# Optimization experiments

Hardware: AMD Instinct MI355X
Metric: run time of the kernel (lower is better)

## Reference

```python
import jax, jax.numpy as jnp
import numpy as np

B, T, D, E = 2, 1653, 512, 8
D_E = D // E
BE = B * E


def setup_inputs() -> dict:
    key = jax.random.key(0)
    ks = jax.random.split(key, 11)
    s = 0.02  # keep linear-layer scale sane
    return {
        "input": jax.random.normal(ks[0], (B, T, D), jnp.float32),
        "Wq": jax.random.normal(ks[1], (D, D), jnp.float32) * s,
        "bq": jax.random.normal(ks[2], (D,), jnp.float32) * s,
        "Wk": jax.random.normal(ks[3], (D, D), jnp.float32) * s,
        "bk": jax.random.normal(ks[4], (D,), jnp.float32) * s,
        "Wv": jax.random.normal(ks[5], (D, D), jnp.float32) * s,
        "bv": jax.random.normal(ks[6], (D,), jnp.float32) * s,
        "Wo": jax.random.normal(ks[7], (D, D), jnp.float32) * s,
        "bo": jax.random.normal(ks[8], (D,), jnp.float32) * s,
        # random 'gaussian orthogonal punishment' matrix (diag(norms) @ blockwise-QR in torch; random here)
        "punish": jax.random.normal(ks[9], (T, T), jnp.float32) * (1.0 / np.sqrt(T)),
        # random tensor produced by torch.nn.init.orthogonal_(att_score) in the source
        "att_orth": jax.random.normal(ks[10], (BE, T, T), jnp.float32) * (1.0 / np.sqrt(T)),
    }


def _learnable_sigmoid(x):
    return 1.2 / (1.0 + jnp.exp(-1.6 * x))


def reference(input, Wq, bq, Wk, bk, Wv, bv, Wo, bo, punish, att_orth):
    # torch nn.Linear: y = x @ W^T + b
    def proj(W, b):
        # [B,T,D] -> permute(0,2,1) -> [B,D,T] -> reshape to [B*E, T, D_E]
        y = jnp.einsum('btd,ed->bte', input, W) + b
        return y.transpose(0, 2, 1).reshape(BE, T, D_E)

    Q = _learnable_sigmoid(proj(Wq, bq))            # [BE, T, D_E] (mask_q is all-ones => no-op)
    K = _learnable_sigmoid(proj(Wk, bk))            # [BE, T, D_E]
    V = proj(Wv, bv)                                # [BE, T, D_E]

    inv_sqrt_T = 1.0 / jnp.sqrt(jnp.float32(T))
    att = jnp.einsum('btd,bsd->bts', Q, K) * inv_sqrt_T  # [BE, T, T]

    # punishment: elementwise mul by broadcast punish matrix, then matmul with
    # the (transposed) random orthogonal tensor: att = (att * P) @ orth^T
    att = (att * punish[None, :, :]) @ att_orth.transpose(0, 2, 1)  # [BE, T, T]

    att = jnp.where(att == 0.0, jnp.float32(-2e20), att)  # masked_fill(att==0, -2e20)

    out = jnp.einsum('bts,bsd->btd', att, V)        # [BE, T, D_E]
    # permute(0,2,1) -> [BE, D_E, T] -> reshape [B, D, T] -> permute -> [B, T, D]
    out = out.transpose(0, 2, 1).reshape(B, D, T).transpose(0, 2, 1)
    return jnp.einsum('btd,ed->bte', out, Wo) + bo   # [B, T, D]
```

## Files before the change

kernel.cpp:

```cpp
#include <hip/hip_runtime.h>

#define TT 1653
#define DD 512
#define BB 2
#define DE 64
#define BEH 16
#define TTILES 26
#define TPAD 1664
#define SQN 26
#define NJC 4
#define MPSTRIDE TPAD

typedef __attribute__((ext_vector_type(8))) short bf16x8;
typedef __attribute__((ext_vector_type(4))) float f32x4;
typedef short bf16x8u __attribute__((ext_vector_type(8), aligned(4)));
typedef float f32x4u  __attribute__((ext_vector_type(4), aligned(4)));

__device__ __forceinline__ short f2bf(float f) {
    union { float f; unsigned u; } v; v.f = f;
    unsigned r = v.u + 0x7fffu + ((v.u >> 16) & 1u);
    return (short)(r >> 16);
}
__device__ __forceinline__ unsigned pack2(float a, float b) {
    return (unsigned)(unsigned short)f2bf(a) | ((unsigned)(unsigned short)f2bf(b) << 16);
}
__device__ __forceinline__ float bf2f(short s) {
    union { unsigned u; float f; } v; v.u = ((unsigned)(unsigned short)s) << 16;
    return v.f;
}
__device__ __forceinline__ bf16x8 ld_frag4(const short* p) {
    bf16x8u v = *(const bf16x8u*)p;
    return (bf16x8)v;
}

__global__ __launch_bounds__(256) void convp2_kernel(
    const float* __restrict__ P, short* __restrict__ Pbf)
{
    const int g = blockIdx.x * 256 + threadIdx.x;
    const int NG4 = TPAD / 4;
    if (g >= TT * NG4) return;
    const int r = g / NG4, c4 = (g - r * NG4) * 4;
    float p0 = 0.f, p1 = 0.f, p2 = 0.f, p3 = 0.f;
    const float* prow = P + (size_t)r * TT;
    if (c4 + 0 < TT) p0 = prow[c4 + 0];
    if (c4 + 1 < TT) p1 = prow[c4 + 1];
    if (c4 + 2 < TT) p2 = prow[c4 + 2];
    if (c4 + 3 < TT) p3 = prow[c4 + 3];
    uint2 o; o.x = pack2(p0, p1); o.y = pack2(p2, p3);
    *(uint2*)(Pbf + (size_t)r * TPAD + c4) = o;
}

__global__ __launch_bounds__(256) void proj2_kernel(
    const float* __restrict__ X,
    const float* __restrict__ W0, const float* __restrict__ b0,
    const float* __restrict__ W1, const float* __restrict__ b1,
    const float* __restrict__ W2, const float* __restrict__ b2,
    short* __restrict__ Y0, short* __restrict__ Y1, short* __restrict__ Y2)
{
    __shared__ short Wsh[64][72];
    __shared__ short Xs[64][72];

    const int tt = blockIdx.x, dt = blockIdx.y, z = blockIdx.z;
    const int b = z / 3, which = z % 3;
    const float* W    = (which == 0) ? W0 : (which == 1) ? W1 : W2;
    const float* bias = (which == 0) ? b0 : (which == 1) ? b1 : b2;
    short* Y          = (which == 0) ? Y0 : (which == 1) ? Y1 : Y2;

    const int t0 = tt * 64, d0 = dt * 64;
    const float* Xb = X + (size_t)b * TT * DD;

    const int tid  = threadIdx.x;
    const int wave = tid >> 6, lane = tid & 63;
    const int quad = lane >> 4, l16 = lane & 15;
    const int srow = tid >> 2, scg = (tid & 3) * 16;

    f32x4 acc[4];
    #pragma unroll
    for (int i = 0; i < 4; ++i) acc[i] = (f32x4){0.f, 0.f, 0.f, 0.f};

    for (int k0 = 0; k0 < DD; k0 += 64) {
        {
            const float* wrow = W + (size_t)(d0 + srow) * DD + k0 + scg;
            float4 w0 = *(const float4*)(wrow);
            float4 w1 = *(const float4*)(wrow + 4);
            float4 w2 = *(const float4*)(wrow + 8);
            float4 w3 = *(const float4*)(wrow + 12);
            uint4 pw0, pw1;
            pw0.x = pack2(w0.x, w0.y); pw0.y = pack2(w0.z, w0.w);
            pw0.z = pack2(w1.x, w1.y); pw0.w = pack2(w1.z, w1.w);
            pw1.x = pack2(w2.x, w2.y); pw1.y = pack2(w2.z, w2.w);
            pw1.z = pack2(w3.x, w3.y); pw1.w = pack2(w3.z, w3.w);

            const int t = t0 + srow;
            float4 x0 = make_float4(0.f,0.f,0.f,0.f), x1 = x0, x2 = x0, x3 = x0;
            if (t < TT) {
                const float* xrow = Xb + (size_t)t * DD + k0 + scg;
                x0 = *(const float4*)(xrow);
                x1 = *(const float4*)(xrow + 4);
                x2 = *(const float4*)(xrow + 8);
                x3 = *(const float4*)(xrow + 12);
            }
            uint4 px0, px1;
            px0.x = pack2(x0.x, x0.y); px0.y = pack2(x0.z, x0.w);
            px0.z = pack2(x1.x, x1.y); px0.w = pack2(x1.z, x1.w);
            px1.x = pack2(x2.x, x2.y); px1.y = pack2(x2.z, x2.w);
            px1.z = pack2(x3.x, x3.y); px1.w = pack2(x3.z, x3.w);

            __syncthreads();
            *(uint4*)&Wsh[srow][scg]     = pw0;
            *(uint4*)&Wsh[srow][scg + 8] = pw1;
            *(uint4*)&Xs[srow][scg]      = px0;
            *(uint4*)&Xs[srow][scg + 8]  = px1;
        }
        __syncthreads();

        #pragma unroll
        for (int ks = 0; ks < 2; ++ks) {
            bf16x8 a = *(const bf16x8*)&Wsh[wave * 16 + l16][ks * 32 + quad * 8];
            #pragma unroll
            for (int nt = 0; nt < 4; ++nt) {
                bf16x8 bb = *(const bf16x8*)&Xs[nt * 16 + l16][ks * 32 + quad * 8];
                acc[nt] = __builtin_amdgcn_mfma_f32_16x16x32_bf16(a, bb, acc[nt], 0, 0, 0);
            }
        }
    }

    #pragma unroll
    for (int nt = 0; nt < 4; ++nt) {
        const int t = t0 + nt * 16 + l16;
        if (t < TT) {
            #pragma unroll
            for (int r = 0; r < 4; ++r) {
                const int d = d0 + wave * 16 + quad * 4 + r;
                float v = acc[nt][r] + bias[d];
                if (which < 2) v = 1.2f / (1.0f + __expf(-1.6f * v));
                Y[((size_t)b * DD + d) * TT + t] = f2bf(v);
            }
        }
    }
}

__global__ __launch_bounds__(256, 6) void ovt4_kernel(
    const float* __restrict__ orth, const short* __restrict__ Vb,
    float* __restrict__ Mpart)
{
    __shared__ short Os[64][66];
    __shared__ short Vs[64][66];

    const int sq = blockIdx.x, be = blockIdx.y, jc = blockIdx.z;
    const int s0 = sq * 64;
    const int jt0 = (jc < 2) ? jc * 7 : 14 + (jc - 2) * 6;
    const int jtn = (jc < 2) ? 7 : 6;

    const float* O  = orth + (size_t)be * TT * TT;
    const short* Vh = Vb + (size_t)be * DE * TT;

    const int tid  = threadIdx.x;
    const int wave = tid >> 6, lane = tid & 63;
    const int quad = lane >> 4, l16 = lane & 15;

    const int c4 = tid & 15;
    const int pr = tid >> 4;
    const int ca = s0 + 4 * c4;
    const bool fastS = (s0 + 64 <= TT);

    f32x4 acc[4];
    #pragma unroll
    for (int i = 0; i < 4; ++i) acc[i] = (f32x4){0.f, 0.f, 0.f, 0.f};

    f32x4u o0a, o0b, o1a, o1b;
    uint2  v0a, v0b, v1a, v1b;

    auto stage_load = [&](int j0) {
        const int jA0 = j0 + 2 * pr;
        const int jA1 = jA0 + 32;
        const int r0  = min(jA0,     TT - 1);
        const int r0b = min(jA0 + 1, TT - 1);
        const int r1  = min(jA1,     TT - 1);
        const int r1b = min(jA1 + 1, TT - 1);
        if (fastS) {
            o0a = *(const f32x4u*)(O + (size_t)r0  * TT + ca);
            o0b = *(const f32x4u*)(O + (size_t)r0b * TT + ca);
            o1a = *(const f32x4u*)(O + (size_t)r1  * TT + ca);
            o1b = *(const f32x4u*)(O + (size_t)r1b * TT + ca);
        } else {
            #pragma unroll
            for (int i = 0; i < 4; ++i) {
                const int col = ca + i;
                const bool cv = (col < TT);
                o0a[i] = cv ? O[(size_t)r0  * TT + col] : 0.f;
                o0b[i] = cv ? O[(size_t)r0b * TT + col] : 0.f;
                o1a[i] = cv ? O[(size_t)r1  * TT + col] : 0.f;
                o1b[i] = cv ? O[(size_t)r1b * TT + col] : 0.f;
            }
        }
        const uint2 z = make_uint2(0u, 0u);
        v0a = (jA0     < TT) ? *(const uint2*)(Vh + (size_t)jA0       * DE + 4 * c4) : z;
        v0b = (jA0 + 1 < TT) ? *(const uint2*)(Vh + (size_t)(jA0 + 1) * DE + 4 * c4) : z;
        v1a = (jA1     < TT) ? *(const uint2*)(Vh + (size_t)jA1       * DE + 4 * c4) : z;
        v1b = (jA1 + 1 < TT) ? *(const uint2*)(Vh + (size_t)(jA1 + 1) * DE + 4 * c4) : z;
    };

    auto lds_write = [&]() {
        #pragma unroll
        for (int i = 0; i < 4; ++i) {
            *(unsigned*)&Os[4 * c4 + i][2 * pr]      = pack2(o0a[i], o0b[i]);
            *(unsigned*)&Os[4 * c4 + i][2 * pr + 32] = pack2(o1a[i], o1b[i]);
        }
        *(unsigned*)&Vs[4 * c4 + 0][2 * pr]      = (v0a.x & 0xffffu) | (v0b.x << 16);
        *(unsigned*)&Vs[4 * c4 + 1][2 * pr]      = (v0a.x >> 16)     | (v0b.x & 0xffff0000u);
        *(unsigned*)&Vs[4 * c4 + 2][2 * pr]      = (v0a.y & 0xffffu) | (v0b.y << 16);
        *(unsigned*)&Vs[4 * c4 + 3][2 * pr]      = (v0a.y >> 16)     | (v0b.y & 0xffff0000u);
        *(unsigned*)&Vs[4 * c4 + 0][2 * pr + 32] = (v1a.x & 0xffffu) | (v1b.x << 16);
        *(unsigned*)&Vs[4 * c4 + 1][2 * pr + 32] = (v1a.x >> 16)     | (v1b.x & 0xffff0000u);
        *(unsigned*)&Vs[4 * c4 + 2][2 * pr + 32] = (v1a.y & 0xffffu) | (v1b.y << 16);
        *(unsigned*)&Vs[4 * c4 + 3][2 * pr + 32] = (v1a.y >> 16)     | (v1b.y & 0xffff0000u);
    };

    stage_load(jt0 * 64);
    for (int t = 0; t < jtn; ++t) {
        if (t) __syncthreads();
        lds_write();
        if (t + 1 < jtn) stage_load((jt0 + t + 1) * 64);
        __syncthreads();
        #pragma unroll
        for (int ks = 0; ks < 2; ++ks) {
            bf16x8 bb = ld_frag4(&Os[wave * 16 + l16][ks * 32 + quad * 8]);
            #pragma unroll
            for (int i = 0; i < 4; ++i) {
                bf16x8 a = ld_frag4(&Vs[i * 16 + l16][ks * 32 + quad * 8]);
                acc[i] = __builtin_amdgcn_mfma_f32_16x16x32_bf16(a, bb, acc[i], 0, 0, 0);
            }
        }
    }

    float* Mp = Mpart + (size_t)(jc * BEH + be) * DE * MPSTRIDE;
    const int s = s0 + wave * 16 + l16;
    #pragma unroll
    for (int i = 0; i < 4; ++i) {
        #pragma unroll
        for (int r = 0; r < 4; ++r) {
            const int d = i * 16 + quad * 4 + r;
            Mp[(size_t)d * MPSTRIDE + s] = acc[i][r];
        }
    }
}

__global__ __launch_bounds__(256) void mreduce_kernel(
    const float* __restrict__ Mpart, short* __restrict__ Mt)
{
    const int g = blockIdx.x * 256 + threadIdx.x;
    const int NG = TPAD / 4;
    if (g >= BEH * DE * NG) return;
    const int bd = g / NG;
    const int s4 = (g - bd * NG) * 4;

    const size_t jstride = (size_t)BEH * DE * MPSTRIDE;
    const float* p = Mpart + (size_t)bd * MPSTRIDE + s4;
    float4 a0 = *(const float4*)(p);
    float4 a1 = *(const float4*)(p + jstride);
    float4 a2 = *(const float4*)(p + 2 * jstride);
    float4 a3 = *(const float4*)(p + 3 * jstride);
    float s0 = a0.x + a1.x + a2.x + a3.x;
    float s1 = a0.y + a1.y + a2.y + a3.y;
    float s2 = a0.z + a1.z + a2.z + a3.z;
    float s3 = a0.w + a1.w + a2.w + a3.w;

    uint2 o;
    o.x = pack2(s0, s1);
    o.y = pack2(s2, s3);
    *(uint2*)(Mt + (size_t)bd * TPAD + s4) = o;
}

__global__ __launch_bounds__(256) void attn2_kernel(
    const short* __restrict__ Qb, const short* __restrict__ Kb,
    const short* __restrict__ Mt, const short* __restrict__ Pbf,
    float* __restrict__ Hbuf)
{
    __shared__ short Qs[64][72];
    __shared__ short Ks[64][72];
    __shared__ short Ms[64][72];
    __shared__ short Wl[64][72];
    __shared__ short Ps[64][72];

    const int it = blockIdx.x, be = blockIdx.y;
    const int b = be >> 3, e = be & 7;
    const int i0 = it * 64;
    const short* Qh = Qb + (size_t)be * DE * TT;
    const short* Kh = Kb + (size_t)be * DE * TT;
    const short* Mh = Mt + (size_t)be * DE * TPAD;

    const int tid  = threadIdx.x;
    const int wave = tid >> 6, lane = tid & 63;
    const int quad = lane >> 4, l16 = lane & 15;

    const float invs = 0.024598297f;

    const int srow = tid >> 2, scg = (tid & 3) * 16;

    {
        const int gi = i0 + srow;
        uint4 z = make_uint4(0u, 0u, 0u, 0u);
        uint4 v0 = z, v1 = z;
        if (gi < TT) {
            v0 = *(const uint4*)(Qh + (size_t)gi * DE + scg);
            v1 = *(const uint4*)(Qh + (size_t)gi * DE + scg + 8);
        }
        *(uint4*)&Qs[srow][scg]     = v0;
        *(uint4*)&Qs[srow][scg + 8] = v1;
    }

    f32x4 out[4];
    #pragma unroll
    for (int i = 0; i < 4; ++i) out[i] = (f32x4){0.f, 0.f, 0.f, 0.f};

    for (int s0 = 0; s0 < TT; s0 += 64) {
        {
            const int gs = s0 + srow;
            uint4 z = make_uint4(0u, 0u, 0u, 0u);
            uint4 k0 = z, k1 = z;
            if (gs < TT) {
                k0 = *(const uint4*)(Kh + (size_t)gs * DE + scg);
                k1 = *(const uint4*)(Kh + (size_t)gs * DE + scg + 8);
            }
            *(uint4*)&Ks[srow][scg]     = k0;
            *(uint4*)&Ks[srow][scg + 8] = k1;

            uint4 m0 = *(const uint4*)(Mh + (size_t)srow * TPAD + s0 + scg);
            uint4 m1 = *(const uint4*)(Mh + (size_t)srow * TPAD + s0 + scg + 8);
            *(uint4*)&Ms[srow][scg]     = m0;
            *(uint4*)&Ms[srow][scg + 8] = m1;

            const int gi = i0 + srow;
            uint4 p0 = z, p1 = z;
            if (gi < TT) {
                p0 = *(const uint4*)(Pbf + (size_t)gi * TPAD + s0 + scg);
                p1 = *(const uint4*)(Pbf + (size_t)gi * TPAD + s0 + scg + 8);
            }
            *(uint4*)&Ps[srow][scg]     = p0;
            *(uint4*)&Ps[srow][scg + 8] = p1;
        }
        __syncthreads();

        f32x4 w[4];
        #pragma unroll
        for (int i = 0; i < 4; ++i) w[i] = (f32x4){0.f, 0.f, 0.f, 0.f};
        #pragma unroll
        for (int ks = 0; ks < 2; ++ks) {
            bf16x8 a = *(const bf16x8*)&Qs[wave * 16 + l16][ks * 32 + quad * 8];
            #pragma unroll
            for (int stile = 0; stile < 4; ++stile) {
                bf16x8 bb = *(const bf16x8*)&Ks[stile * 16 + l16][ks * 32 + quad * 8];
                w[stile] = __builtin_amdgcn_mfma_f32_16x16x32_bf16(a, bb, w[stile], 0, 0, 0);
            }
        }

        #pragma unroll
        for (int stile = 0; stile < 4; ++stile) {
            const int sl = stile * 16 + l16;
            #pragma unroll
            for (int r = 0; r < 4; ++r) {
                const int il = wave * 16 + quad * 4 + r;
                float v = w[stile][r] * invs * bf2f(Ps[il][sl]);
                Wl[il][sl] = f2bf(v);
            }
        }

        #pragma unroll
        for (int ks = 0; ks < 2; ++ks) {
            bf16x8 a = *(const bf16x8*)&Wl[wave * 16 + l16][ks * 32 + quad * 8];
            #pragma unroll
            for (int dt = 0; dt < 4; ++dt) {
                bf16x8 bb = *(const bf16x8*)&Ms[dt * 16 + l16][ks * 32 + quad * 8];
                out[dt] = __builtin_amdgcn_mfma_f32_16x16x32_bf16(a, bb, out[dt], 0, 0, 0);
            }
        }
        __syncthreads();
    }

    #pragma unroll
    for (int dt = 0; dt < 4; ++dt) {
        const int d = dt * 16 + l16;
        #pragma unroll
        for (int r = 0; r < 4; ++r) {
            const int gi = i0 + wave * 16 + quad * 4 + r;
            if (gi < TT)
                Hbuf[((size_t)b * TT + gi) * DD + e * 64 + d] = out[dt][r];
        }
    }
}

__global__ __launch_bounds__(256) void oproj_kernel(
    const float* __restrict__ H, const float* __restrict__ Wo,
    const float* __restrict__ bo, float* __restrict__ out)
{
    __shared__ float Hs[16][68];
    __shared__ float Ns[16][68];

    const int tt = blockIdx.x, nt = blockIdx.y, b = blockIdx.z;
    const int t0 = tt * 64, n0 = nt * 64;
    const float* Hb = H + (size_t)b * TT * DD;

    const int tid = threadIdx.x;
    const int tx = tid & 15, ty = tid >> 4;
    const int lrow = tid >> 2, lq = tid & 3;
    const int trow = t0 + lrow;

    float acc[4][4] = {};

    for (int k0 = 0; k0 < DD; k0 += 16) {
        float4 hv = make_float4(0.f, 0.f, 0.f, 0.f);
        if (trow < TT)
            hv = *(const float4*)(Hb + (size_t)trow * DD + k0 + lq*4);
        float4 wv = *(const float4*)(Wo + (size_t)(n0 + lrow) * DD + k0 + lq*4);
        __syncthreads();
        Hs[lq*4+0][lrow] = hv.x; Hs[lq*4+1][lrow] = hv.y;
        Hs[lq*4+2][lrow] = hv.z; Hs[lq*4+3][lrow] = hv.w;
        Ns[lq*4+0][lrow] = wv.x; Ns[lq*4+1][lrow] = wv.y;
        Ns[lq*4+2][lrow] = wv.z; Ns[lq*4+3][lrow] = wv.w;
        __syncthreads();
        #pragma unroll
        for (int k = 0; k < 16; ++k) {
            float4 a4 = *(const float4*)(&Hs[k][ty*4]);
            float4 c4 = *(const float4*)(&Ns[k][tx*4]);
            float a[4] = {a4.x, a4.y, a4.z, a4.w};
            float c[4] = {c4.x, c4.y, c4.z, c4.w};
            #pragma unroll
            for (int i = 0; i < 4; ++i)
                #pragma unroll
                for (int j = 0; j < 4; ++j)
                    acc[i][j] = fmaf(a[i], c[j], acc[i][j]);
        }
        __syncthreads();
    }

    #pragma unroll
    for (int i = 0; i < 4; ++i) {
        const int t = t0 + ty*4 + i;
        if (t < TT) {
            float4 v;
            v.x = acc[i][0] + bo[n0 + tx*4 + 0];
            v.y = acc[i][1] + bo[n0 + tx*4 + 1];
            v.z = acc[i][2] + bo[n0 + tx*4 + 2];
            v.w = acc[i][3] + bo[n0 + tx*4 + 3];
            *(float4*)(out + ((size_t)b * TT + t) * DD + n0 + tx*4) = v;
        }
    }
}

extern "C" void kernel_launch(void* const* d_in, const int* in_sizes, int n_in,
                              void* d_out, int out_size, void* d_ws, size_t ws_size,
                              hipStream_t stream)
{
    (void)in_sizes; (void)n_in; (void)out_size; (void)ws_size;

    const float* X    = (const float*)d_in[0];
    const float* Wq   = (const float*)d_in[1];
    const float* bq   = (const float*)d_in[2];
    const float* Wk   = (const float*)d_in[3];
    const float* bk   = (const float*)d_in[4];
    const float* Wv   = (const float*)d_in[5];
    const float* bv   = (const float*)d_in[6];
    const float* Wo   = (const float*)d_in[7];
    const float* bo   = (const float*)d_in[8];
    const float* P    = (const float*)d_in[9];
    const float* orth = (const float*)d_in[10];
    float* out = (float*)d_out;

    char* ws = (char*)d_ws;
    const size_t SZH = (size_t)BB * DD * TT * sizeof(short);
    short* Qb  = (short*)(ws);
    short* Kb  = (short*)(ws + SZH);
    short* Vb  = (short*)(ws + 2 * SZH);
    short* Mtb = (short*)(ws + 3 * SZH);
    short* Pbf = (short*)(ws + 3 * SZH + (size_t)BEH * DE * TPAD * sizeof(short));
    char*  after_p = ws + 3 * SZH + (size_t)BEH * DE * TPAD * sizeof(short)
                        + (size_t)TT * TPAD * sizeof(short);
    float* Mpart = (float*)after_p;
    float* Hbuf  = (float*)after_p;

    dim3 blk(256);

    convp2_kernel<<<dim3((TT * (TPAD / 4) + 255) / 256), blk, 0, stream>>>(P, Pbf);

    dim3 g1(TTILES, DD / 64, BB * 3);
    proj2_kernel<<<g1, blk, 0, stream>>>(X, Wq, bq, Wk, bk, Wv, bv, Qb, Kb, Vb);

    dim3 g2(SQN, BEH, NJC);
    ovt4_kernel<<<g2, blk, 0, stream>>>(orth, Vb, Mpart);

    dim3 gr((BEH * DE * (TPAD / 4) + 255) / 256);
    mreduce_kernel<<<gr, blk, 0, stream>>>(Mpart, Mtb);

    dim3 g3(TTILES, BEH);
    attn2_kernel<<<g3, blk, 0, stream>>>(Qb, Kb, Mtb, Pbf, Hbuf);

    dim3 g4(TTILES, DD / 64, BB);
    oproj_kernel<<<g4, blk, 0, stream>>>(Hbuf, Wo, bo, out);
}
```

Baseline: 409.4 us.

## Add register double-buffered prefetch to projection, OV and attention kernels

Each of the three main kernels now loads the next K-tile from global memory into registers while computing on the current tile. The OV kernel moves to a two-stage register ping-pong and relaxes launch bounds to 4 waves per SIMD. The attention kernel also gains two-stage register staging and drops the separate Wl LDS buffer by writing the scaled scores back into Ps. The aim is to hide global load latency and cut LDS footprint, at the cost of higher register pressure and lower occupancy.

```diff
diff --git a/kernel.cpp b/kernel.cpp
--- a/kernel.cpp
+++ b/kernel.cpp
@@ -13,7 +13,6 @@
 
 typedef __attribute__((ext_vector_type(8))) short bf16x8;
 typedef __attribute__((ext_vector_type(4))) float f32x4;
-typedef short bf16x8u __attribute__((ext_vector_type(8), aligned(4)));
 typedef float f32x4u  __attribute__((ext_vector_type(4), aligned(4)));
 
 __device__ __forceinline__ short f2bf(float f) {
@@ -27,10 +26,6 @@
 __device__ __forceinline__ float bf2f(short s) {
     union { unsigned u; float f; } v; v.u = ((unsigned)(unsigned short)s) << 16;
     return v.f;
-}
-__device__ __forceinline__ bf16x8 ld_frag4(const short* p) {
-    bf16x8u v = *(const bf16x8u*)p;
-    return (bf16x8)v;
 }
 
 __global__ __launch_bounds__(256) void convp2_kernel(
@@ -50,15 +45,15 @@
     *(uint2*)(Pbf + (size_t)r * TPAD + c4) = o;
 }
 
-__global__ __launch_bounds__(256) void proj2_kernel(
+__global__ __launch_bounds__(256) void proj3_kernel(
     const float* __restrict__ X,
     const float* __restrict__ W0, const float* __restrict__ b0,
     const float* __restrict__ W1, const float* __restrict__ b1,
     const float* __restrict__ W2, const float* __restrict__ b2,
     short* __restrict__ Y0, short* __restrict__ Y1, short* __restrict__ Y2)
 {
-    __shared__ short Wsh[64][72];
-    __shared__ short Xs[64][72];
+    __shared__ __align__(16) short Wsh[64][72];
+    __shared__ __align__(16) short Xs[64][72];
 
     const int tt = blockIdx.x, dt = blockIdx.y, z = blockIdx.z;
     const int b = z / 3, which = z % 3;
@@ -78,40 +73,45 @@
     #pragma unroll
     for (int i = 0; i < 4; ++i) acc[i] = (f32x4){0.f, 0.f, 0.f, 0.f};
 
+    float4 w0, w1, w2, w3, x0, x1, x2, x3;
+
+    auto stage = [&](int k0) {
+        const float* wrow = W + (size_t)(d0 + srow) * DD + k0 + scg;
+        w0 = *(const float4*)(wrow);
+        w1 = *(const float4*)(wrow + 4);
+        w2 = *(const float4*)(wrow + 8);
+        w3 = *(const float4*)(wrow + 12);
+        const int t = t0 + srow;
+        x0 = make_float4(0.f,0.f,0.f,0.f); x1 = x0; x2 = x0; x3 = x0;
+        if (t < TT) {
+            const float* xrow = Xb + (size_t)t * DD + k0 + scg;
+            x0 = *(const float4*)(xrow);
+            x1 = *(const float4*)(xrow + 4);
+            x2 = *(const float4*)(xrow + 8);
+            x3 = *(const float4*)(xrow + 12);
+        }
+    };
+    auto lds_write = [&]() {
+        uint4 pw0, pw1, px0, px1;
+        pw0.x = pack2(w0.x, w0.y); pw0.y = pack2(w0.z, w0.w);
+        pw0.z = pack2(w1.x, w1.y); pw0.w = pack2(w1.z, w1.w);
+        pw1.x = pack2(w2.x, w2.y); pw1.y = pack2(w2.z, w2.w);
+        pw1.z = pack2(w3.x, w3.y); pw1.w = pack2(w3.z, w3.w);
+        px0.x = pack2(x0.x, x0.y); px0.y = pack2(x0.z, x0.w);
+        px0.z = pack2(x1.x, x1.y); px0.w = pack2(x1.z, x1.w);
+        px1.x = pack2(x2.x, x2.y); px1.y = pack2(x2.z, x2.w);
+        px1.z = pack2(x3.x, x3.y); px1.w = pack2(x3.z, x3.w);
+        *(uint4*)&Wsh[srow][scg]     = pw0;
+        *(uint4*)&Wsh[srow][scg + 8] = pw1;
+        *(uint4*)&Xs[srow][scg]      = px0;
+        *(uint4*)&Xs[srow][scg + 8]  = px1;
+    };
+
+    stage(0);
     for (int k0 = 0; k0 < DD; k0 += 64) {
-        {
-            const float* wrow = W + (size_t)(d0 + srow) * DD + k0 + scg;
-            float4 w0 = *(const float4*)(wrow);
-            float4 w1 = *(const float4*)(wrow + 4);
-            float4 w2 = *(const float4*)(wrow + 8);
-            float4 w3 = *(const float4*)(wrow + 12);
-            uint4 pw0, pw1;
-            pw0.x = pack2(w0.x, w0.y); pw0.y = pack2(w0.z, w0.w);
-            pw0.z = pack2(w1.x, w1.y); pw0.w = pack2(w1.z, w1.w);
-            pw1.x = pack2(w2.x, w2.y); pw1.y = pack2(w2.z, w2.w);
-            pw1.z = pack2(w3.x, w3.y); pw1.w = pack2(w3.z, w3.w);
-
-            const int t = t0 + srow;
-            float4 x0 = make_float4(0.f,0.f,0.f,0.f), x1 = x0, x2 = x0, x3 = x0;
-            if (t < TT) {
-                const float* xrow = Xb + (size_t)t * DD + k0 + scg;
-                x0 = *(const float4*)(xrow);
-                x1 = *(const float4*)(xrow + 4);
-                x2 = *(const float4*)(xrow + 8);
-                x3 = *(const float4*)(xrow + 12);
-            }
-            uint4 px0, px1;
-            px0.x = pack2(x0.x, x0.y); px0.y = pack2(x0.z, x0.w);
-            px0.z = pack2(x1.x, x1.y); px0.w = pack2(x1.z, x1.w);
-            px1.x = pack2(x2.x, x2.y); px1.y = pack2(x2.z, x2.w);
-            px1.z = pack2(x3.x, x3.y); px1.w = pack2(x3.z, x3.w);
-
-            __syncthreads();
-            *(uint4*)&Wsh[srow][scg]     = pw0;
-            *(uint4*)&Wsh[srow][scg + 8] = pw1;
-            *(uint4*)&Xs[srow][scg]      = px0;
-            *(uint4*)&Xs[srow][scg + 8]  = px1;
-        }
+        if (k0) __syncthreads();
+        lds_write();
+        if (k0 + 64 < DD) stage(k0 + 64);
         __syncthreads();
 
         #pragma unroll
@@ -140,12 +140,17 @@
     }
 }
 
-__global__ __launch_bounds__(256, 6) void ovt4_kernel(
+struct OVStage {
+    f32x4u o0a, o0b, o1a, o1b;
+    uint2  v0a, v0b, v1a, v1b;
+};
+
+__global__ __launch_bounds__(256, 4) void ovt5_kernel(
     const float* __restrict__ orth, const short* __restrict__ Vb,
     float* __restrict__ Mpart)
 {
-    __shared__ short Os[64][66];
-    __shared__ short Vs[64][66];
+    __shared__ __align__(16) short Os[64][72];
+    __shared__ __align__(16) short Vs[64][72];
 
     const int sq = blockIdx.x, be = blockIdx.y, jc = blockIdx.z;
     const int s0 = sq * 64;
@@ -159,78 +164,88 @@
     const int wave = tid >> 6, lane = tid & 63;
     const int quad = lane >> 4, l16 = lane & 15;
 
-    const int c4 = tid & 15;
-    const int pr = tid >> 4;
-    const int ca = s0 + 4 * c4;
+    const int p  = tid & 15;
+    const int sc = tid >> 4;
+    const int ca = s0 + 4 * sc;
     const bool fastS = (s0 + 64 <= TT);
 
     f32x4 acc[4];
     #pragma unroll
     for (int i = 0; i < 4; ++i) acc[i] = (f32x4){0.f, 0.f, 0.f, 0.f};
 
-    f32x4u o0a, o0b, o1a, o1b;
-    uint2  v0a, v0b, v1a, v1b;
-
-    auto stage_load = [&](int j0) {
-        const int jA0 = j0 + 2 * pr;
-        const int jA1 = jA0 + 32;
-        const int r0  = min(jA0,     TT - 1);
-        const int r0b = min(jA0 + 1, TT - 1);
-        const int r1  = min(jA1,     TT - 1);
-        const int r1b = min(jA1 + 1, TT - 1);
+    auto stage_load = [&](OVStage& S, int j0) {
+        const int jA = j0 + 2 * p;
+        const int r0  = min(jA,      TT - 1);
+        const int r0b = min(jA + 1,  TT - 1);
+        const int r1  = min(jA + 32, TT - 1);
+        const int r1b = min(jA + 33, TT - 1);
         if (fastS) {
-            o0a = *(const f32x4u*)(O + (size_t)r0  * TT + ca);
-            o0b = *(const f32x4u*)(O + (size_t)r0b * TT + ca);
-            o1a = *(const f32x4u*)(O + (size_t)r1  * TT + ca);
-            o1b = *(const f32x4u*)(O + (size_t)r1b * TT + ca);
+            S.o0a = *(const f32x4u*)(O + (size_t)r0  * TT + ca);
+            S.o0b = *(const f32x4u*)(O + (size_t)r0b * TT + ca);
+            S.o1a = *(const f32x4u*)(O + (size_t)r1  * TT + ca);
+            S.o1b = *(const f32x4u*)(O + (size_t)r1b * TT + ca);
         } else {
             #pragma unroll
             for (int i = 0; i < 4; ++i) {
                 const int col = ca + i;
                 const bool cv = (col < TT);
-                o0a[i] = cv ? O[(size_t)r0  * TT + col] : 0.f;
-                o0b[i] = cv ? O[(size_t)r0b * TT + col] : 0.f;
-                o1a[i] = cv ? O[(size_t)r1  * TT + col] : 0.f;
-                o1b[i] = cv ? O[(size_t)r1b * TT + col] : 0.f;
+                S.o0a[i] = cv ? O[(size_t)r0  * TT + col] : 0.f;
+                S.o0b[i] = cv ? O[(size_t)r0b * TT + col] : 0.f;
+                S.o1a[i] = cv ? O[(size_t)r1  * TT + col] : 0.f;
+                S.o1b[i] = cv ? O[(size_t)r1b * TT + col] : 0.f;
             }
         }
         const uint2 z = make_uint2(0u, 0u);
-        v0a = (jA0     < TT) ? *(const uint2*)(Vh + (size_t)jA0       * DE + 4 * c4) : z;
-        v0b = (jA0 + 1 < TT) ? *(const uint2*)(Vh + (size_t)(jA0 + 1) * DE + 4 * c4) : z;
-        v1a = (jA1     < TT) ? *(const uint2*)(Vh + (size_t)jA1       * DE + 4 * c4) : z;
-        v1b = (jA1 + 1 < TT) ? *(const uint2*)(Vh + (size_t)(jA1 + 1) * DE + 4 * c4) : z;
-    };
-
-    auto lds_write = [&]() {
+        S.v0a = (jA      < TT) ? *(const uint2*)(Vh + (size_t)jA       * DE + 4 * sc) : z;
+        S.v0b = (jA + 1  < TT) ? *(const uint2*)(Vh + (size_t)(jA + 1) * DE + 4 * sc) : z;
+        S.v1a = (jA + 32 < TT) ? *(const uint2*)(Vh + (size_t)(jA + 32)* DE + 4 * sc) : z;
+        S.v1b = (jA + 33 < TT) ? *(const uint2*)(Vh + (size_t)(jA + 33)* DE + 4 * sc) : z;
+    };
+
+    auto lds_write = [&](const OVStage& S) {
         #pragma unroll
         for (int i = 0; i < 4; ++i) {
-            *(unsigned*)&Os[4 * c4 + i][2 * pr]      = pack2(o0a[i], o0b[i]);
-            *(unsigned*)&Os[4 * c4 + i][2 * pr + 32] = pack2(o1a[i], o1b[i]);
-        }
-        *(unsigned*)&Vs[4 * c4 + 0][2 * pr]      = (v0a.x & 0xffffu) | (v0b.x << 16);
-        *(unsigned*)&Vs[4 * c4 + 1][2 * pr]      = (v0a.x >> 16)     | (v0b.x & 0xffff0000u);
-        *(unsigned*)&Vs[4 * c4 + 2][2 * pr]      = (v0a.y & 0xffffu) | (v0b.y << 16);
-        *(unsigned*)&Vs[4 * c4 + 3][2 * pr]      = (v0a.y >> 16)     | (v0b.y & 0xffff0000u);
-        *(unsigned*)&Vs[4 * c4 + 0][2 * pr + 32] = (v1a.x & 0xffffu) | (v1b.x << 16);
-        *(unsigned*)&Vs[4 * c4 + 1][2 * pr + 32] = (v1a.x >> 16)     | (v1b.x & 0xffff0000u);
-        *(unsigned*)&Vs[4 * c4 + 2][2 * pr + 32] = (v1a.y & 0xffffu) | (v1b.y << 16);
-        *(unsigned*)&Vs[4 * c4 + 3][2 * pr + 32] = (v1a.y >> 16)     | (v1b.y & 0xffff0000u);
-    };
-
-    stage_load(jt0 * 64);
-    for (int t = 0; t < jtn; ++t) {
+            *(unsigned*)&Os[4 * sc + i][2 * p]      = pack2(S.o0a[i], S.o0b[i]);
+            *(unsigned*)&Os[4 * sc + i][2 * p + 32] = pack2(S.o1a[i], S.o1b[i]);
+        }
+        *(unsigned*)&Vs[4 * sc + 0][2 * p]      = (S.v0a.x & 0xffffu) | (S.v0b.x << 16);
+        *(unsigned*)&Vs[4 * sc + 1][2 * p]      = (S.v0a.x >> 16)     | (S.v0b.x & 0xffff0000u);
+        *(unsigned*)&Vs[4 * sc + 2][2 * p]      = (S.v0a.y & 0xffffu) | (S.v0b.y << 16);
+        *(unsigned*)&Vs[4 * sc + 3][2 * p]      = (S.v0a.y >> 16)     | (S.v0b.y & 0xffff0000u);
+        *(unsigned*)&Vs[4 * sc + 0][2 * p + 32] = (S.v1a.x & 0xffffu) | (S.v1b.x << 16);
+        *(unsigned*)&Vs[4 * sc + 1][2 * p + 32] = (S.v1a.x >> 16)     | (S.v1b.x & 0xffff0000u);
+        *(unsigned*)&Vs[4 * sc + 2][2 * p + 32] = (S.v1a.y & 0xffffu) | (S.v1b.y << 16);
+        *(unsigned*)&Vs[4 * sc + 3][2 * p + 32] = (S.v1a.y >> 16)     | (S.v1b.y & 0xffff0000u);
+    };
+
+    auto mfma_tile = [&]() {
+        #pragma unroll
+        for (int ks = 0; ks < 2; ++ks) {
+            bf16x8 bb = *(const bf16x8*)&Os[wave * 16 + l16][ks * 32 + quad * 8];
+            #pragma unroll
+            for (int i = 0; i < 4; ++i) {
+                bf16x8 a = *(const bf16x8*)&Vs[i * 16 + l16][ks * 32 + quad * 8];
+                acc[i] = __builtin_amdgcn_mfma_f32_16x16x32_bf16(a, bb, acc[i], 0, 0, 0);
+            }
+        }
+    };
+
+    OVStage sA, sB;
+    stage_load(sA, (jt0 + 0) * 64);
+    if (jtn > 1) stage_load(sB, (jt0 + 1) * 64);
+
+    for (int t = 0; t < jtn; t += 2) {
         if (t) __syncthreads();
-        lds_write();
-        if (t + 1 < jtn) stage_load((jt0 + t + 1) * 64);
-        __syncthreads();
-        #pragma unroll
-        for (int ks = 0; ks < 2; ++ks) {
-            bf16x8 bb = ld_frag4(&Os[wave * 16 + l16][ks * 32 + quad * 8]);
-            #pragma unroll
-            for (int i = 0; i < 4; ++i) {
-                bf16x8 a = ld_frag4(&Vs[i * 16 + l16][ks * 32 + quad * 8]);
-                acc[i] = __builtin_amdgcn_mfma_f32_16x16x32_bf16(a, bb, acc[i], 0, 0, 0);
-            }
+        lds_write(sA);
+        if (t + 2 < jtn) stage_load(sA, (jt0 + t + 2) * 64);
+        __syncthreads();
+        mfma_tile();
+        if (t + 1 < jtn) {
+            __syncthreads();
+            lds_write(sB);
+            if (t + 3 < jtn) stage_load(sB, (jt0 + t + 3) * 64);
+            __syncthreads();
+            mfma_tile();
         }
     }
 
@@ -272,16 +287,19 @@
     *(uint2*)(Mt + (size_t)bd * TPAD + s4) = o;
 }
 
-__global__ __launch_bounds__(256) void attn2_kernel(
+struct AStage {
+    uint4 k0, k1, m0, m1, p0, p1;
+};
+
+__global__ __launch_bounds__(256, 4) void attn3_kernel(
     const short* __restrict__ Qb, const short* __restrict__ Kb,
     const short* __restrict__ Mt, const short* __restrict__ Pbf,
     float* __restrict__ Hbuf)
 {
-    __shared__ short Qs[64][72];
-    __shared__ short Ks[64][72];
-    __shared__ short Ms[64][72];
-    __shared__ short Wl[64][72];
-    __shared__ short Ps[64][72];
+    __shared__ __align__(16) short Qs[64][72];
+    __shared__ __align__(16) short Ks[64][72];
+    __shared__ __align__(16) short Ms[64][72];
+    __shared__ __align__(16) short Ps[64][72];
 
     const int it = blockIdx.x, be = blockIdx.y;
     const int b = be >> 3, e = be & 7;
@@ -297,12 +315,13 @@
     const float invs = 0.024598297f;
 
     const int srow = tid >> 2, scg = (tid & 3) * 16;
+    const int gi = i0 + srow;
+    const bool giv = (gi < TT);
 
     {
-        const int gi = i0 + srow;
         uint4 z = make_uint4(0u, 0u, 0u, 0u);
         uint4 v0 = z, v1 = z;
-        if (gi < TT) {
+        if (giv) {
             v0 = *(const uint4*)(Qh + (size_t)gi * DE + scg);
             v1 = *(const uint4*)(Qh + (size_t)gi * DE + scg + 8);
         }
@@ -314,34 +333,33 @@
     #pragma unroll
     for (int i = 0; i < 4; ++i) out[i] = (f32x4){0.f, 0.f, 0.f, 0.f};
 
-    for (int s0 = 0; s0 < TT; s0 += 64) {
-        {
-            const int gs = s0 + srow;
-            uint4 z = make_uint4(0u, 0u, 0u, 0u);
-            uint4 k0 = z, k1 = z;
-            if (gs < TT) {
-                k0 = *(const uint4*)(Kh + (size_t)gs * DE + scg);
-                k1 = *(const uint4*)(Kh + (size_t)gs * DE + scg + 8);
-            }
-            *(uint4*)&Ks[srow][scg]     = k0;
-            *(uint4*)&Ks[srow][scg + 8] = k1;
-
-            uint4 m0 = *(const uint4*)(Mh + (size_t)srow * TPAD + s0 + scg);
-            uint4 m1 = *(const uint4*)(Mh + (size_t)srow * TPAD + s0 + scg + 8);
-            *(uint4*)&Ms[srow][scg]     = m0;
-            *(uint4*)&Ms[srow][scg + 8] = m1;
-
-            const int gi = i0 + srow;
-            uint4 p0 = z, p1 = z;
-            if (gi < TT) {
-                p0 = *(const uint4*)(Pbf + (size_t)gi * TPAD + s0 + scg);
-                p1 = *(const uint4*)(Pbf + (size_t)gi * TPAD + s0 + scg + 8);
-            }
-            *(uint4*)&Ps[srow][scg]     = p0;
-            *(uint4*)&Ps[srow][scg + 8] = p1;
-        }
-        __syncthreads();
-
+    auto stage_regs = [&](AStage& S, int s0) {
+        const uint4 z = make_uint4(0u, 0u, 0u, 0u);
+        const int gs = s0 + srow;
+        S.k0 = z; S.k1 = z;
+        if (gs < TT) {
+            S.k0 = *(const uint4*)(Kh + (size_t)gs * DE + scg);
+            S.k1 = *(const uint4*)(Kh + (size_t)gs * DE + scg + 8);
+        }
+        S.m0 = *(const uint4*)(Mh + (size_t)srow * TPAD + s0 + scg);
+        S.m1 = *(const uint4*)(Mh + (size_t)srow * TPAD + s0 + scg + 8);
+        S.p0 = z; S.p1 = z;
+        if (giv) {
+            S.p0 = *(const uint4*)(Pbf + (size_t)gi * TPAD + s0 + scg);
+            S.p1 = *(const uint4*)(Pbf + (size_t)gi * TPAD + s0 + scg + 8);
+        }
+    };
+
+    auto lds_write = [&](const AStage& S) {
+        *(uint4*)&Ks[srow][scg]     = S.k0;
+        *(uint4*)&Ks[srow][scg + 8] = S.k1;
+        *(uint4*)&Ms[srow][scg]     = S.m0;
+        *(uint4*)&Ms[srow][scg + 8] = S.m1;
+        *(uint4*)&Ps[srow][scg]     = S.p0;
+        *(uint4*)&Ps[srow][scg + 8] = S.p1;
+    };
+
+    auto compute = [&]() {
         f32x4 w[4];
         #pragma unroll
         for (int i = 0; i < 4; ++i) w[i] = (f32x4){0.f, 0.f, 0.f, 0.f};
@@ -362,20 +380,36 @@
             for (int r = 0; r < 4; ++r) {
                 const int il = wave * 16 + quad * 4 + r;
                 float v = w[stile][r] * invs * bf2f(Ps[il][sl]);
-                Wl[il][sl] = f2bf(v);
+                Ps[il][sl] = f2bf(v);
             }
         }
 
         #pragma unroll
         for (int ks = 0; ks < 2; ++ks) {
-            bf16x8 a = *(const bf16x8*)&Wl[wave * 16 + l16][ks * 32 + quad * 8];
+            bf16x8 a = *(const bf16x8*)&Ps[wave * 16 + l16][ks * 32 + quad * 8];
             #pragma unroll
             for (int dt = 0; dt < 4; ++dt) {
                 bf16x8 bb = *(const bf16x8*)&Ms[dt * 16 + l16][ks * 32 + quad * 8];
                 out[dt] = __builtin_amdgcn_mfma_f32_16x16x32_bf16(a, bb, out[dt], 0, 0, 0);
             }
         }
-        __syncthreads();
+    };
+
+    AStage sA, sB;
+    stage_regs(sA, 0);
+    stage_regs(sB, 64);
+
+    for (int tt = 0; tt < TTILES; tt += 2) {
+        if (tt) __syncthreads();
+        lds_write(sA);
+        if (tt + 2 < TTILES) stage_regs(sA, (tt + 2) * 64);
+        __syncthreads();
+        compute();
+        __syncthreads();
+        lds_write(sB);
+        if (tt + 3 < TTILES) stage_regs(sB, (tt + 3) * 64);
+        __syncthreads();
+        compute();
     }
 
     #pragma unroll
@@ -383,9 +417,9 @@
         const int d = dt * 16 + l16;
         #pragma unroll
         for (int r = 0; r < 4; ++r) {
-            const int gi = i0 + wave * 16 + quad * 4 + r;
-            if (gi < TT)
-                Hbuf[((size_t)b * TT + gi) * DD + e * 64 + d] = out[dt][r];
+            const int go = i0 + wave * 16 + quad * 4 + r;
+            if (go < TT)
+                Hbuf[((size_t)b * TT + go) * DD + e * 64 + d] = out[dt][r];
         }
     }
 }
@@ -484,16 +518,16 @@
     convp2_kernel<<<dim3((TT * (TPAD / 4) + 255) / 256), blk, 0, stream>>>(P, Pbf);
 
     dim3 g1(TTILES, DD / 64, BB * 3);
-    proj2_kernel<<<g1, blk, 0, stream>>>(X, Wq, bq, Wk, bk, Wv, bv, Qb, Kb, Vb);
+    proj3_kernel<<<g1, blk, 0, stream>>>(X, Wq, bq, Wk, bk, Wv, bv, Qb, Kb, Vb);
 
     dim3 g2(SQN, BEH, NJC);
-    ovt4_kernel<<<g2, blk, 0, stream>>>(orth, Vb, Mpart);
+    ovt5_kernel<<<g2, blk, 0, stream>>>(orth, Vb, Mpart);
 
     dim3 gr((BEH * DE * (TPAD / 4) + 255) / 256);
     mreduce_kernel<<<gr, blk, 0, stream>>>(Mpart, Mtb);
 
     dim3 g3(TTILES, BEH);
-    attn2_kernel<<<g3, blk, 0, stream>>>(Qb, Kb, Mtb, Pbf, Hbuf);
+    attn3_kernel<<<g3, blk, 0, stream>>>(Qb, Kb, Mtb, Pbf, Hbuf);
 
     dim3 g4(TTILES, DD / 64, BB);
     oproj_kernel<<<g4, blk, 0, stream>>>(Hbuf, Wo, bo, out);
```

Result: no change. 408.0 us (-0.3%).
